# Performance work log

Hardware: AMD Instinct MI355X
Metric: run time of the kernel (lower is better)

The kernel has to match this reference:

```python
import jax, jax.numpy as jnp
import numpy as np
from jax.scipy.special import logsumexp

B, L, M, D = 8192, 1024, 128, 2  # batch, hilbert.size, bond dim, local_size
MACHINE_POW = 2


def setup_inputs() -> dict:
    key = jax.random.key(0)
    k1, k2 = jax.random.split(key)
    # configurations in the zero-magnetization sector: each row is a permutation
    # of L//2 zeros and L//2 ones (constrained HomogeneousHilbert)
    base = jnp.tile(jnp.arange(D, dtype=jnp.int32), L // D)  # (L,)
    inputs = jax.vmap(lambda k: jax.random.permutation(k, base))(jax.random.split(k1, B))
    # variational parameters epsilon: (local_size, M, size); centered at 1 so the
    # length-L multiplicative cache chain stays in fp32 range
    epsilon = 1.0 + 0.02 * jax.random.normal(k2, (D, M, L), dtype=jnp.float32)
    return {"inputs": inputs, "epsilon": epsilon}


def _conditionals(inputs, epsilon):
    # inputs: (B, L) int in [0, D); epsilon: (D, M, L)
    Bn, Ln = inputs.shape
    Dn, Mn, _ = epsilon.shape
    half = Ln // 2

    def scan_fun(carry, index):
        cache, n_spins = carry                       # (B, D, M), (B, D)
        prev = inputs[:, (index - 1) % Ln]           # (B,) previous-site state
        params_i = epsilon[:, :, index]              # (D, M)
        # irregular gather: cache[b, prev[b], :]
        gathered = jnp.take_along_axis(cache, prev[:, None, None], axis=1)[:, 0, :]  # (B, M)
        prods = params_i[None, :, :] * gathered[:, None, :]  # (B, D, M)
        log_psi = jnp.sum(prods, axis=-1)            # (B, D) sum over bond dim
        n_spins = jnp.where(index > 0,
                            n_spins + jax.nn.one_hot(prev, Dn, dtype=jnp.int32),
                            n_spins)
        # zero-magnetization renormalization: -inf once a local state is exhausted
        renorm = jnp.log(jnp.heaviside((half - n_spins).astype(log_psi.dtype), 0.0))
        return (prods, n_spins), log_psi + renorm

    cache0 = jnp.ones((Bn, Dn, Mn), epsilon.dtype)
    n0 = jnp.zeros((Bn, Dn), jnp.int32)
    _, log_psi = jax.lax.scan(scan_fun, (cache0, n0), jnp.arange(Ln))
    return jnp.transpose(log_psi, (1, 0, 2))  # (B, L, D)


def reference(inputs, epsilon):
    lp = _conditionals(inputs, epsilon)  # (B, L, D)
    # normalize conditionals over local states (machine_pow = 2)
    lp = lp - (1.0 / MACHINE_POW) * logsumexp(MACHINE_POW * lp, axis=-1, keepdims=True)
    # pick the log-conditional of the actual configuration at each site
    sel = jnp.take_along_axis(lp, inputs[:, :, None], axis=2)[:, :, 0]  # (B, L)
    # n_symm = 1 (default apply_symmetries): symmetrized logsumexp is identity
    return jnp.sum(sel, axis=1)  # (B,) log_psi
```

## Files before the change

kernel.cpp:

```cpp
#include <hip/hip_runtime.h>

typedef unsigned long long u64;
typedef unsigned int uint32;
typedef short short8 __attribute__((ext_vector_type(8)));
typedef float f32x4 __attribute__((ext_vector_type(4)));

#define B_N 8192
#define L_N 1024
#define M_N 128
#define C_N 16
#define CH_N 64
#define HALF_N 512
#define SL 20
#define ROWF (8 * SL)

#define OFF_W    0
#define OFF_R    0x80000
#define OFF_BITS 0x100000
#define OFF_LR   0x208000
#define OFF_RQ   0x248000

__device__ __forceinline__ unsigned short f32_bf16(float f) {
    union { float f; unsigned u; } x; x.f = f;
    unsigned u = x.u + 0x7FFFu + ((x.u >> 16) & 1u);
    return (unsigned short)(u >> 16);
}
__device__ __forceinline__ float bf16lo(uint32 w) {
    union { unsigned u; float f; } x; x.u = w << 16; return x.f;
}
__device__ __forceinline__ float bf16hi(uint32 w) {
    union { unsigned u; float f; } x; x.u = w & 0xFFFF0000u; return x.f;
}

__global__ __launch_bounds__(256) void k_pack(const int* __restrict__ inp, u64* __restrict__ bits) {
    int g = blockIdx.x * 256 + threadIdx.x;
    int v = inp[g];
    u64 m = __ballot(v != 0);
    if ((threadIdx.x & 63) == 0) bits[g >> 6] = m;
}

__global__ __launch_bounds__(64) void k_eps(const float* __restrict__ eps,
        float* __restrict__ w, float* __restrict__ r, unsigned short* __restrict__ lrT) {
    int m = blockIdx.x, lane = threadIdx.x;
    const float* e0 = eps + (size_t)m * L_N + lane * 16;
    const float* e1 = eps + (size_t)(M_N + m) * L_N + lane * 16;
    float a[16], b[16];
    #pragma unroll
    for (int j = 0; j < 16; j += 4) {
        *(float4*)&a[j] = *(const float4*)&e0[j];
        *(float4*)&b[j] = *(const float4*)&e1[j];
    }
    float local = 1.f;
    #pragma unroll
    for (int j = 0; j < 16; ++j) local *= a[j];
    float sc = local;
    #pragma unroll
    for (int d = 1; d < 64; d <<= 1) {
        float up = __shfl_up(sc, d);
        if (lane >= d) sc *= up;
    }
    float prev = __shfl_up(sc, 1);
    float E = (lane == 0) ? 1.f : prev;
    int i0 = lane * 16;
    #pragma unroll
    for (int j = 0; j < 16; ++j) {
        float rat = b[j] / a[j];
        w[(size_t)(i0 + j) * M_N + m] = E * (a[j] - b[j]);
        r[(size_t)(i0 + j) * M_N + m] = rat;
        lrT[(size_t)m * L_N + i0 + j] = f32_bf16(__log2f(rat));
        E *= a[j];
    }
}

__global__ __launch_bounds__(256) void k_slogsum(const u64* __restrict__ bits,
        const unsigned short* __restrict__ lrT, unsigned short* __restrict__ Rq) {
    int c = blockIdx.x & (C_N - 1);
    int bt2 = blockIdx.x >> 4;
    int wid = threadIdx.x >> 6, lane = threadIdx.x & 63;
    int btile = bt2 * 2 + (wid >> 1);
    int mbase = (wid & 1) * 64;
    int col = lane & 15, quad = lane >> 4;
    int b_row = btile * 16 + col;

    u64 wv = bits[(size_t)b_row * 16 + c];
    short8 a0, a1;
    #pragma unroll
    for (int j = 0; j < 8; ++j) {
        a0[j] = (short)((((wv >> (quad * 8 + j)) & 1) != 0) ? 0x3F80 : 0);
        a1[j] = (short)((((wv >> (32 + quad * 8 + j)) & 1) != 0) ? 0x3F80 : 0);
    }
    #pragma unroll
    for (int mt = 0; mt < 4; ++mt) {
        int m = mbase + mt * 16 + col;
        const unsigned short* bp = lrT + (size_t)m * L_N + c * 64 + quad * 8;
        union { uint4 u; short8 s; } bf0, bf1;
        bf0.u = *(const uint4*)bp;
        bf1.u = *(const uint4*)(bp + 32);
        f32x4 acc = (f32x4){0.f, 0.f, 0.f, 0.f};
        acc = __builtin_amdgcn_mfma_f32_16x16x32_bf16(a0, bf0.s, acc, 0, 0, 0);
        acc = __builtin_amdgcn_mfma_f32_16x16x32_bf16(a1, bf1.s, acc, 0, 0, 0);
        #pragma unroll
        for (int reg = 0; reg < 4; ++reg) {
            int b = btile * 16 + quad * 4 + reg;
            Rq[((size_t)c * B_N + b) * M_N + mbase + mt * 16 + col] = f32_bf16(acc[reg]);
        }
    }
}

__global__ __launch_bounds__(256) void k_prefix(unsigned short* __restrict__ Rq) {
    int t = blockIdx.x * 256 + threadIdx.x;
    int b = t >> 7, m = t & 127;
    float p = 0.f;
    for (int c = 0; c < C_N; ++c) {
        size_t idx = ((size_t)c * B_N + b) * M_N + m;
        union { unsigned u; float f; } x; x.u = ((unsigned)Rq[idx]) << 16;
        Rq[idx] = f32_bf16(exp2f(p));
        p += x.f;
    }
}

__global__ __launch_bounds__(256, 4) void k_main(const u64* __restrict__ bits,
        const float* __restrict__ w, const float* __restrict__ r,
        const unsigned short* __restrict__ Rq, float* __restrict__ out) {
    __shared__ float wbuf[32 * ROWF];
    __shared__ float rbuf[32 * ROWF];
    int c = blockIdx.x & (C_N - 1);
    int bblk = blockIdx.x >> 4;
    int lane = threadIdx.x & 63, wid = threadIdx.x >> 6;
    int s = lane & 7, g = lane >> 3;
    int b0 = bblk * 128 + wid * 32 + g * 4;
    int b_own = b0 + (s & 3);

    float R[4][16];
    #pragma unroll
    for (int nb = 0; nb < 4; ++nb) {
        const uint4* src = (const uint4*)(Rq + ((size_t)c * B_N + (b0 + nb)) * M_N + s * 16);
        #pragma unroll
        for (int u_ = 0; u_ < 2; ++u_) {
            uint4 pv = src[u_];
            R[nb][u_ * 8 + 0] = bf16lo(pv.x); R[nb][u_ * 8 + 1] = bf16hi(pv.x);
            R[nb][u_ * 8 + 2] = bf16lo(pv.y); R[nb][u_ * 8 + 3] = bf16hi(pv.y);
            R[nb][u_ * 8 + 4] = bf16lo(pv.z); R[nb][u_ * 8 + 5] = bf16hi(pv.z);
            R[nb][u_ * 8 + 6] = bf16lo(pv.w); R[nb][u_ * 8 + 7] = bf16hi(pv.w);
        }
    }
    int n1 = 0;
    for (int k = 0; k < c; ++k) n1 += __popcll(bits[(size_t)b_own * 16 + k]);
    int n0 = c * CH_N - n1;

    float sum = 0.f;
    for (int h = 0; h < 2; ++h) {
        __syncthreads();
        const float4* srcw = (const float4*)(w + ((size_t)c * CH_N + h * 32) * M_N);
        const float4* srcr = (const float4*)(r + ((size_t)c * CH_N + h * 32) * M_N);
        for (int t = threadIdx.x; t < 32 * 32; t += 256) {
            int i = t >> 5, mq = t & 31;
            int dst = i * ROWF + (mq >> 2) * SL + (mq & 3) * 4;
            *(float4*)&wbuf[dst] = srcw[t];
            *(float4*)&rbuf[dst] = srcr[t];
        }
        __syncthreads();

        uint32 wh[4];
        #pragma unroll
        for (int nb = 0; nb < 4; ++nb)
            wh[nb] = (uint32)(bits[(size_t)(b0 + nb) * 16 + c] >> (h * 32));
        uint32 owa = (s & 1) ? wh[1] : wh[0];
        uint32 owb = (s & 1) ? wh[3] : wh[2];
        uint32 ow = (s & 2) ? owb : owa;

        for (int tt = 0; tt < 32; ++tt) {
            int base = tt * ROWF + s * SL;
            float4 va = *(const float4*)&wbuf[base];
            float4 vb = *(const float4*)&wbuf[base + 4];
            float4 vc = *(const float4*)&wbuf[base + 8];
            float4 vd = *(const float4*)&wbuf[base + 12];
            float d[4];
            #pragma unroll
            for (int nb = 0; nb < 4; ++nb) {
                d[nb] = R[nb][0] * va.x + R[nb][1] * va.y + R[nb][2] * va.z + R[nb][3] * va.w
                      + R[nb][4] * vb.x + R[nb][5] * vb.y + R[nb][6] * vb.z + R[nb][7] * vb.w
                      + R[nb][8] * vc.x + R[nb][9] * vc.y + R[nb][10] * vc.z + R[nb][11] * vc.w
                      + R[nb][12] * vd.x + R[nb][13] * vd.y + R[nb][14] * vd.z + R[nb][15] * vd.w;
            }
            #pragma unroll
            for (int nb = 0; nb < 4; ++nb) {
                d[nb] += __shfl_xor(d[nb], 1);
                d[nb] += __shfl_xor(d[nb], 2);
                d[nb] += __shfl_xor(d[nb], 4);
            }
            float t01 = (s & 1) ? d[1] : d[0];
            float t23 = (s & 1) ? d[3] : d[2];
            float Dv = (s & 2) ? t23 : t01;

            int sbit = (ow >> tt) & 1;
            bool valid = (n0 < HALF_N) && (n1 < HALF_N);
            float ad = fabsf(Dv);
            float contr = -fmaxf(sbit ? Dv : -Dv, 0.f)
                          - 0.5f * __logf(1.f + __expf(-2.f * ad));
            sum += valid ? contr : 0.f;
            n1 += sbit; n0 += 1 - sbit;

            float4 ra = *(const float4*)&rbuf[base];
            float4 rb = *(const float4*)&rbuf[base + 4];
            float4 rc = *(const float4*)&rbuf[base + 8];
            float4 rd = *(const float4*)&rbuf[base + 12];
            #pragma unroll
            for (int nb = 0; nb < 4; ++nb) {
                if ((wh[nb] >> tt) & 1) {
                    R[nb][0] *= ra.x;  R[nb][1] *= ra.y;  R[nb][2] *= ra.z;  R[nb][3] *= ra.w;
                    R[nb][4] *= rb.x;  R[nb][5] *= rb.y;  R[nb][6] *= rb.z;  R[nb][7] *= rb.w;
                    R[nb][8] *= rc.x;  R[nb][9] *= rc.y;  R[nb][10] *= rc.z; R[nb][11] *= rc.w;
                    R[nb][12] *= rd.x; R[nb][13] *= rd.y; R[nb][14] *= rd.z; R[nb][15] *= rd.w;
                }
            }
        }
    }
    if (s < 4) atomicAdd(&out[b_own], sum);
}

extern "C" void kernel_launch(void* const* d_in, const int* in_sizes, int n_in,
                              void* d_out, int out_size, void* d_ws, size_t ws_size,
                              hipStream_t stream) {
    const int*   inputs  = (const int*)d_in[0];
    const float* epsilon = (const float*)d_in[1];
    float* out = (float*)d_out;

    char* ws = (char*)d_ws;
    float* w_tab  = (float*)(ws + OFF_W);
    float* r_tab  = (float*)(ws + OFF_R);
    u64*   bits   = (u64*)  (ws + OFF_BITS);
    unsigned short* lrT = (unsigned short*)(ws + OFF_LR);
    unsigned short* Rq  = (unsigned short*)(ws + OFF_RQ);

    k_pack<<<(B_N * L_N) / 256, 256, 0, stream>>>(inputs, bits);
    k_eps<<<M_N, 64, 0, stream>>>(epsilon, w_tab, r_tab, lrT);
    hipMemsetAsync(d_out, 0, B_N * sizeof(float), stream);
    k_slogsum<<<(B_N / 32) * C_N, 256, 0, stream>>>(bits, lrT, Rq);
    k_prefix<<<(B_N * M_N) / 256, 256, 0, stream>>>(Rq);
    k_main<<<(B_N / 128) * C_N, 256, 0, stream>>>(bits, w_tab, r_tab, Rq, out);
}
```

Before: 202.3 us.

## Fuse chunk log-sum and prefix kernels; use packed FP32 math and shuffle-select reduction

The separate chunk log-sum MFMA kernel and the exp2 prefix-scan kernel are merged into one kernel. It keeps running MFMA accumulators across the 16 chunks and writes exp2 of the running prefix directly. This removes a write and re-read of the Rq intermediate and one launch. The main kernel's dot products and ratio updates now use v_pk_fma_f32 and v_pk_mul_f32 on float2 pairs. The final shuffle reduction selects the batch row before its last xor-shuffle, saving three shuffles per step. The fused kernel has fewer blocks (B/16) and serial chunk iterations, which may reduce parallelism.

After: 199.1 us. About the same (-1.6%).

```diff
diff --git a/kernel.cpp b/kernel.cpp
--- a/kernel.cpp
+++ b/kernel.cpp
@@ -32,6 +32,17 @@
     union { unsigned u; float f; } x; x.u = w & 0xFFFF0000u; return x.f;
 }
 
+__device__ __forceinline__ float2 pk_fma(float2 a, float2 b, float2 c) {
+    float2 d;
+    asm("v_pk_fma_f32 %0, %1, %2, %3" : "=v"(d) : "v"(a), "v"(b), "v"(c));
+    return d;
+}
+__device__ __forceinline__ float2 pk_mul(float2 a, float2 b) {
+    float2 d;
+    asm("v_pk_mul_f32 %0, %1, %2" : "=v"(d) : "v"(a), "v"(b));
+    return d;
+}
+
 __global__ __launch_bounds__(256) void k_pack(const int* __restrict__ inp, u64* __restrict__ bits) {
     int g = blockIdx.x * 256 + threadIdx.x;
     int v = inp[g];
@@ -72,50 +83,45 @@
     }
 }
 
-__global__ __launch_bounds__(256) void k_slogsum(const u64* __restrict__ bits,
+__global__ __launch_bounds__(256) void k_slog2(const u64* __restrict__ bits,
         const unsigned short* __restrict__ lrT, unsigned short* __restrict__ Rq) {
-    int c = blockIdx.x & (C_N - 1);
-    int bt2 = blockIdx.x >> 4;
-    int wid = threadIdx.x >> 6, lane = threadIdx.x & 63;
-    int btile = bt2 * 2 + (wid >> 1);
-    int mbase = (wid & 1) * 64;
+    int btile = blockIdx.x;
+    int mq = threadIdx.x >> 6, lane = threadIdx.x & 63;
     int col = lane & 15, quad = lane >> 4;
     int b_row = btile * 16 + col;
-
-    u64 wv = bits[(size_t)b_row * 16 + c];
-    short8 a0, a1;
-    #pragma unroll
-    for (int j = 0; j < 8; ++j) {
-        a0[j] = (short)((((wv >> (quad * 8 + j)) & 1) != 0) ? 0x3F80 : 0);
-        a1[j] = (short)((((wv >> (32 + quad * 8 + j)) & 1) != 0) ? 0x3F80 : 0);
-    }
-    #pragma unroll
-    for (int mt = 0; mt < 4; ++mt) {
-        int m = mbase + mt * 16 + col;
-        const unsigned short* bp = lrT + (size_t)m * L_N + c * 64 + quad * 8;
-        union { uint4 u; short8 s; } bf0, bf1;
-        bf0.u = *(const uint4*)bp;
-        bf1.u = *(const uint4*)(bp + 32);
-        f32x4 acc = (f32x4){0.f, 0.f, 0.f, 0.f};
-        acc = __builtin_amdgcn_mfma_f32_16x16x32_bf16(a0, bf0.s, acc, 0, 0, 0);
-        acc = __builtin_amdgcn_mfma_f32_16x16x32_bf16(a1, bf1.s, acc, 0, 0, 0);
-        #pragma unroll
-        for (int reg = 0; reg < 4; ++reg) {
-            int b = btile * 16 + quad * 4 + reg;
-            Rq[((size_t)c * B_N + b) * M_N + mbase + mt * 16 + col] = f32_bf16(acc[reg]);
-        }
-    }
-}
-
-__global__ __launch_bounds__(256) void k_prefix(unsigned short* __restrict__ Rq) {
-    int t = blockIdx.x * 256 + threadIdx.x;
-    int b = t >> 7, m = t & 127;
-    float p = 0.f;
+    const u64* brow = bits + (size_t)b_row * 16;
+
+    f32x4 cum[2];
+    cum[0] = (f32x4){0.f, 0.f, 0.f, 0.f};
+    cum[1] = (f32x4){0.f, 0.f, 0.f, 0.f};
+
     for (int c = 0; c < C_N; ++c) {
-        size_t idx = ((size_t)c * B_N + b) * M_N + m;
-        union { unsigned u; float f; } x; x.u = ((unsigned)Rq[idx]) << 16;
-        Rq[idx] = f32_bf16(exp2f(p));
-        p += x.f;
+        #pragma unroll
+        for (int mt = 0; mt < 2; ++mt) {
+            #pragma unroll
+            for (int reg = 0; reg < 4; ++reg) {
+                int b = btile * 16 + quad * 4 + reg;
+                int m = mq * 32 + mt * 16 + col;
+                Rq[((size_t)c * B_N + b) * M_N + m] = f32_bf16(exp2f(cum[mt][reg]));
+            }
+        }
+        u64 wv = brow[c];
+        short8 a0, a1;
+        #pragma unroll
+        for (int j = 0; j < 8; ++j) {
+            a0[j] = (short)((((wv >> (quad * 8 + j)) & 1) != 0) ? 0x3F80 : 0);
+            a1[j] = (short)((((wv >> (32 + quad * 8 + j)) & 1) != 0) ? 0x3F80 : 0);
+        }
+        #pragma unroll
+        for (int mt = 0; mt < 2; ++mt) {
+            int m = mq * 32 + mt * 16 + col;
+            const unsigned short* bp = lrT + (size_t)m * L_N + c * 64 + quad * 8;
+            union { uint4 u; short8 s; } bf0, bf1;
+            bf0.u = *(const uint4*)bp;
+            bf1.u = *(const uint4*)(bp + 32);
+            cum[mt] = __builtin_amdgcn_mfma_f32_16x16x32_bf16(a0, bf0.s, cum[mt], 0, 0, 0);
+            cum[mt] = __builtin_amdgcn_mfma_f32_16x16x32_bf16(a1, bf1.s, cum[mt], 0, 0, 0);
+        }
     }
 }
 
@@ -131,17 +137,17 @@
     int b0 = bblk * 128 + wid * 32 + g * 4;
     int b_own = b0 + (s & 3);
 
-    float R[4][16];
+    float2 R2[4][8];
     #pragma unroll
     for (int nb = 0; nb < 4; ++nb) {
         const uint4* src = (const uint4*)(Rq + ((size_t)c * B_N + (b0 + nb)) * M_N + s * 16);
         #pragma unroll
         for (int u_ = 0; u_ < 2; ++u_) {
             uint4 pv = src[u_];
-            R[nb][u_ * 8 + 0] = bf16lo(pv.x); R[nb][u_ * 8 + 1] = bf16hi(pv.x);
-            R[nb][u_ * 8 + 2] = bf16lo(pv.y); R[nb][u_ * 8 + 3] = bf16hi(pv.y);
-            R[nb][u_ * 8 + 4] = bf16lo(pv.z); R[nb][u_ * 8 + 5] = bf16hi(pv.z);
-            R[nb][u_ * 8 + 6] = bf16lo(pv.w); R[nb][u_ * 8 + 7] = bf16hi(pv.w);
+            R2[nb][u_ * 4 + 0] = make_float2(bf16lo(pv.x), bf16hi(pv.x));
+            R2[nb][u_ * 4 + 1] = make_float2(bf16lo(pv.y), bf16hi(pv.y));
+            R2[nb][u_ * 4 + 2] = make_float2(bf16lo(pv.z), bf16hi(pv.z));
+            R2[nb][u_ * 4 + 3] = make_float2(bf16lo(pv.w), bf16hi(pv.w));
         }
     }
     int n1 = 0;
@@ -154,8 +160,8 @@
         const float4* srcw = (const float4*)(w + ((size_t)c * CH_N + h * 32) * M_N);
         const float4* srcr = (const float4*)(r + ((size_t)c * CH_N + h * 32) * M_N);
         for (int t = threadIdx.x; t < 32 * 32; t += 256) {
-            int i = t >> 5, mq = t & 31;
-            int dst = i * ROWF + (mq >> 2) * SL + (mq & 3) * 4;
+            int i = t >> 5, mqd = t & 31;
+            int dst = i * ROWF + (mqd >> 2) * SL + (mqd & 3) * 4;
             *(float4*)&wbuf[dst] = srcw[t];
             *(float4*)&rbuf[dst] = srcr[t];
         }
@@ -171,27 +177,31 @@
 
         for (int tt = 0; tt < 32; ++tt) {
             int base = tt * ROWF + s * SL;
-            float4 va = *(const float4*)&wbuf[base];
-            float4 vb = *(const float4*)&wbuf[base + 4];
-            float4 vc = *(const float4*)&wbuf[base + 8];
-            float4 vd = *(const float4*)&wbuf[base + 12];
+            const float2* wp = (const float2*)&wbuf[base];
+            float2 w2[8];
+            #pragma unroll
+            for (int j = 0; j < 8; ++j) w2[j] = wp[j];
+
             float d[4];
             #pragma unroll
             for (int nb = 0; nb < 4; ++nb) {
-                d[nb] = R[nb][0] * va.x + R[nb][1] * va.y + R[nb][2] * va.z + R[nb][3] * va.w
-                      + R[nb][4] * vb.x + R[nb][5] * vb.y + R[nb][6] * vb.z + R[nb][7] * vb.w
-                      + R[nb][8] * vc.x + R[nb][9] * vc.y + R[nb][10] * vc.z + R[nb][11] * vc.w
-                      + R[nb][12] * vd.x + R[nb][13] * vd.y + R[nb][14] * vd.z + R[nb][15] * vd.w;
+                float2 acc = pk_mul(R2[nb][0], w2[0]);
+                #pragma unroll
+                for (int j = 1; j < 8; ++j) acc = pk_fma(R2[nb][j], w2[j], acc);
+                d[nb] = acc.x + acc.y;
             }
             #pragma unroll
             for (int nb = 0; nb < 4; ++nb) {
                 d[nb] += __shfl_xor(d[nb], 1);
                 d[nb] += __shfl_xor(d[nb], 2);
-                d[nb] += __shfl_xor(d[nb], 4);
-            }
-            float t01 = (s & 1) ? d[1] : d[0];
-            float t23 = (s & 1) ? d[3] : d[2];
-            float Dv = (s & 2) ? t23 : t01;
+            }
+            int sb3 = s & 3;
+            float sel = d[0];
+            if (sb3 == 1) sel = d[1];
+            if (sb3 == 2) sel = d[2];
+            if (sb3 == 3) sel = d[3];
+            sel += __shfl_xor(sel, 4);
+            float Dv = sel;
 
             int sbit = (ow >> tt) & 1;
             bool valid = (n0 < HALF_N) && (n1 < HALF_N);
@@ -201,17 +211,15 @@
             sum += valid ? contr : 0.f;
             n1 += sbit; n0 += 1 - sbit;
 
-            float4 ra = *(const float4*)&rbuf[base];
-            float4 rb = *(const float4*)&rbuf[base + 4];
-            float4 rc = *(const float4*)&rbuf[base + 8];
-            float4 rd = *(const float4*)&rbuf[base + 12];
+            const float2* rp = (const float2*)&rbuf[base];
+            float2 r2[8];
+            #pragma unroll
+            for (int j = 0; j < 8; ++j) r2[j] = rp[j];
             #pragma unroll
             for (int nb = 0; nb < 4; ++nb) {
                 if ((wh[nb] >> tt) & 1) {
-                    R[nb][0] *= ra.x;  R[nb][1] *= ra.y;  R[nb][2] *= ra.z;  R[nb][3] *= ra.w;
-                    R[nb][4] *= rb.x;  R[nb][5] *= rb.y;  R[nb][6] *= rb.z;  R[nb][7] *= rb.w;
-                    R[nb][8] *= rc.x;  R[nb][9] *= rc.y;  R[nb][10] *= rc.z; R[nb][11] *= rc.w;
-                    R[nb][12] *= rd.x; R[nb][13] *= rd.y; R[nb][14] *= rd.z; R[nb][15] *= rd.w;
+                    #pragma unroll
+                    for (int j = 0; j < 8; ++j) R2[nb][j] = pk_mul(R2[nb][j], r2[j]);
                 }
             }
         }
@@ -236,7 +244,6 @@
     k_pack<<<(B_N * L_N) / 256, 256, 0, stream>>>(inputs, bits);
     k_eps<<<M_N, 64, 0, stream>>>(epsilon, w_tab, r_tab, lrT);
     hipMemsetAsync(d_out, 0, B_N * sizeof(float), stream);
-    k_slogsum<<<(B_N / 32) * C_N, 256, 0, stream>>>(bits, lrT, Rq);
-    k_prefix<<<(B_N * M_N) / 256, 256, 0, stream>>>(Rq);
+    k_slog2<<<B_N / 16, 256, 0, stream>>>(bits, lrT, Rq);
     k_main<<<(B_N / 128) * C_N, 256, 0, stream>>>(bits, w_tab, r_tab, Rq, out);
 }
```
